# Performance work log

Measured on AMD Instinct MI355X. Metric: run time of the kernel, lower is better.

The kernel has to match this reference:

```python
import jax, jax.numpy as jnp
import numpy as np

B, H, T, D = 4, 16, 4096, 64
N_TASKS, K_LEN = 8, 128


def setup_inputs() -> dict:
    key = jax.random.key(0)
    ks = jax.random.split(key, 6)
    x = jax.random.normal(ks[0], (B, H, T, D), dtype=jnp.float32)
    q = jax.random.normal(ks[1], (B, H, T, D), dtype=jnp.float32)
    kv_k = jax.random.normal(ks[2], (N_TASKS, H, K_LEN, D), dtype=jnp.float32)
    kv_v = jax.random.normal(ks[3], (N_TASKS, H, K_LEN, D), dtype=jnp.float32)
    gates = jax.random.uniform(ks[4], (N_TASKS,), dtype=jnp.float32)
    trk_id = jax.random.randint(ks[5], (B, T), 0, N_TASKS, dtype=jnp.int64)
    return {"x": x, "q": q, "kv_k": kv_k, "kv_v": kv_v, "gates": gates, "trk_id": trk_id}


def reference(x, q, kv_k, kv_v, gates, trk_id):
    # Faithful to ICLAdaptor.fn: per-task SDPA of each token's query against
    # that task's (k, v) adaptor memory, scaled by a learned gate, scattered
    # back by trk_id, residual-added to x. Ragged torch gather/scatter is
    # expressed as masked per-task dense attention (small fixed n_tasks loop).
    d = q.shape[-1]
    scale = jnp.asarray(1.0, q.dtype) / jnp.sqrt(jnp.asarray(d, q.dtype))
    n_tasks = kv_k.shape[0]
    dx = jnp.zeros_like(q)
    for i in range(n_tasks):
        # scores: [b, h, t, k_len]
        s = jnp.einsum('bhtd,hkd->bhtk', q, kv_k[i]) * scale
        a = jax.nn.softmax(s, axis=-1)
        o = jnp.einsum('bhtk,hkd->bhtd', a, kv_v[i]) * gates[i]
        mask = (trk_id == i)[:, None, :, None]  # [b,1,t,1]
        dx = dx + jnp.where(mask, o, jnp.zeros((), o.dtype))
    return x + dx
```

## Files before the change

### kernel.cpp

```cpp
#include <hip/hip_runtime.h>

#define B_   4
#define H_   16
#define T_   4096
#define D_   64
#define KL_  128
#define NT_  8
#define NTOK (B_ * T_)
#define CAP  4096

typedef __bf16 bf16;
typedef __attribute__((ext_vector_type(8))) __bf16 bf16x8;
typedef __attribute__((ext_vector_type(4))) __bf16 bf16x4;
typedef __attribute__((ext_vector_type(4))) float  floatx4;
typedef __attribute__((ext_vector_type(4))) unsigned int uint4v;

__global__ void zero_counts_k(int* __restrict__ ws) {
    if (threadIdx.x < NT_) ws[threadIdx.x] = 0;
}

__global__ void scatter_tokens_k(const int* __restrict__ trk, int* __restrict__ ws) {
    int* counts = ws;
    int* bucket = ws + NT_;
    int idx  = blockIdx.x * blockDim.x + threadIdx.x;
    int lane = threadIdx.x & 63;
    int task = (idx < NTOK) ? trk[idx] : -1;
    unsigned long long mymask = 0ull;
    int myCnt = 0;
#pragma unroll
    for (int i = 0; i < NT_; i++) {
        unsigned long long m = __ballot(task == i);
        if (task == i) mymask = m;
        if (lane == i) myCnt = (int)__popcll(m);
    }
    int b0 = 0;
    if (lane < NT_) b0 = atomicAdd(&counts[lane], myCnt);
    int myBase = __shfl(b0, (task < 0) ? 0 : task);
    if (idx < NTOK) {
        int pos = myBase + (int)__popcll(mymask & ((1ull << lane) - 1ull));
        bucket[task * CAP + pos] = idx;
    }
}

static __device__ __forceinline__ unsigned pk_bf16(float a, float b) {
    unsigned short ua = __builtin_bit_cast(unsigned short, (bf16)a);
    unsigned short ub = __builtin_bit_cast(unsigned short, (bf16)b);
    return (unsigned)ua | ((unsigned)ub << 16);
}

__global__ __launch_bounds__(256) void attn_k(
    const float* __restrict__ q,   const float* __restrict__ kvk,
    const float* __restrict__ kvv, const float* __restrict__ gates,
    const float* __restrict__ x,   float* __restrict__ out,
    const int* __restrict__ ws)
{
    __shared__ bf16 Kl[KL_ * D_];
    __shared__ bf16 Vt[D_ * KL_];

    const int task = blockIdx.z, h = blockIdx.y, chunk = blockIdx.x;
    const int cnt = ws[task];
    if (cnt == 0) return;
    const int* bucket = ws + NT_ + task * CAP;
    const float gate = gates[task];

    {
        const size_t kvbase = (size_t)(task * H_ + h) * (KL_ * D_ / 4);
        const float4* kf = (const float4*)kvk + kvbase;
        const float4* vf = (const float4*)kvv + kvbase;
#pragma unroll
        for (int it = 0; it < 8; it++) {
            int ii = it * 256 + threadIdx.x;
            int k = ii >> 4, d4 = ii & 15;
            float4 a = kf[ii];
            bf16x4 w; w[0]=(bf16)a.x; w[1]=(bf16)a.y; w[2]=(bf16)a.z; w[3]=(bf16)a.w;
            *(bf16x4*)&Kl[(k << 6) + (((d4 >> 1) ^ (k & 7)) << 3) + ((d4 & 1) << 2)] = w;
            float4 v = vf[ii];
            int d0 = d4 << 2, ku = k >> 3, kl = k & 7;
            Vt[(d0+0)*128 + ((ku ^ ((d0+0)&7))<<3) + kl] = (bf16)v.x;
            Vt[(d0+1)*128 + ((ku ^ ((d0+1)&7))<<3) + kl] = (bf16)v.y;
            Vt[(d0+2)*128 + ((ku ^ ((d0+2)&7))<<3) + kl] = (bf16)v.z;
            Vt[(d0+3)*128 + ((ku ^ ((d0+3)&7))<<3) + kl] = (bf16)v.w;
        }
    }
    __syncthreads();

    const int lane = threadIdx.x & 63;
    const int wave = threadIdx.x >> 6;
    const int c = lane & 15, quad = lane >> 4;
    const int cswz = c & 7;
    const int src_h0 = c + 16 * (( 2 * quad     ) & 3);
    const int src_h1 = c + 16 * (( 2 * quad + 1 ) & 3);
    const bool hiSel = ((quad >> 1) & 1) != 0;

    for (int ts = chunk * 4 + wave; ts * 16 < cnt; ts += 64) {
        const int slotc = ts * 16 + c;
        const int tokc  = bucket[slotc < cnt ? slotc : cnt - 1];

        bf16x8 aq[2];
        {
            int bb = tokc >> 12, tt = tokc & (T_ - 1);
            const float4* qf = (const float4*)q + ((size_t)((bb * H_ + h) * T_ + tt) * (D_ / 4));
#pragma unroll
            for (int dc = 0; dc < 2; dc++) {
                float4 f0 = qf[dc * 8 + quad * 2];
                float4 f1 = qf[dc * 8 + quad * 2 + 1];
                aq[dc][0]=(bf16)f0.x; aq[dc][1]=(bf16)f0.y; aq[dc][2]=(bf16)f0.z; aq[dc][3]=(bf16)f0.w;
                aq[dc][4]=(bf16)f1.x; aq[dc][5]=(bf16)f1.y; aq[dc][6]=(bf16)f1.z; aq[dc][7]=(bf16)f1.w;
            }
        }

        floatx4 sc[8];
#pragma unroll
        for (int nt = 0; nt < 8; nt++) { floatx4 z = {0.f,0.f,0.f,0.f}; sc[nt] = z; }
        __builtin_amdgcn_s_setprio(1);
#pragma unroll
        for (int dc = 0; dc < 2; dc++) {
#pragma unroll
            for (int nt = 0; nt < 8; nt++) {
                bf16x8 ak = *(const bf16x8*)&Kl[((nt * 16 + c) << 6) + (((4 * dc + quad) ^ cswz) << 3)];
                sc[nt] = __builtin_amdgcn_mfma_f32_16x16x32_bf16(ak, aq[dc], sc[nt], 0, 0, 0);
            }
        }
        __builtin_amdgcn_s_setprio(0);

        float m = -1e30f;
#pragma unroll
        for (int nt = 0; nt < 8; nt++)
#pragma unroll
            for (int r = 0; r < 4; r++) m = fmaxf(m, sc[nt][r]);
        m = fmaxf(m, __shfl_xor(m, 16));
        m = fmaxf(m, __shfl_xor(m, 32));
        float sum = 0.f;
#pragma unroll
        for (int nt = 0; nt < 8; nt++)
#pragma unroll
            for (int r = 0; r < 4; r++) {
                float p = exp2f((sc[nt][r] - m) * 0.18033688011112042f);
                sc[nt][r] = p;
                sum += p;
            }
        sum += __shfl_xor(sum, 16);
        sum += __shfl_xor(sum, 32);
        float ginv = gate / sum;

        unsigned pkv[8][2];
#pragma unroll
        for (int nt = 0; nt < 8; nt++) {
            pkv[nt][0] = pk_bf16(sc[nt][0], sc[nt][1]);
            pkv[nt][1] = pk_bf16(sc[nt][2], sc[nt][3]);
        }

        int base_r[4];
        float xr[4][4];
#pragma unroll
        for (int r = 0; r < 4; r++) {
            int tok = __shfl(tokc, quad * 4 + r);
            int b2 = tok >> 12, t2 = tok & (T_ - 1);
            base_r[r] = ((b2 * H_ + h) * T_ + t2) * D_;
            if (ts * 16 + quad * 4 + r < cnt) {
#pragma unroll
                for (int dt = 0; dt < 4; dt++) xr[r][dt] = x[base_r[r] + dt * 16 + c];
            }
        }

        floatx4 acc[4];
#pragma unroll
        for (int dt = 0; dt < 4; dt++) { floatx4 z = {0.f,0.f,0.f,0.f}; acc[dt] = z; }
#pragma unroll
        for (int kc = 0; kc < 4; kc++) {
            unsigned e0 = pkv[2*kc][0],   e1 = pkv[2*kc][1];
            unsigned o0 = pkv[2*kc+1][0], o1 = pkv[2*kc+1][1];
            unsigned a0e = __shfl(e0, src_h0), a0o = __shfl(o0, src_h0);
            unsigned a1e = __shfl(e1, src_h0), a1o = __shfl(o1, src_h0);
            unsigned a2e = __shfl(e0, src_h1), a2o = __shfl(o0, src_h1);
            unsigned a3e = __shfl(e1, src_h1), a3o = __shfl(o1, src_h1);
            uint4v uw;
            uw[0] = hiSel ? a0o : a0e;
            uw[1] = hiSel ? a1o : a1e;
            uw[2] = hiSel ? a2o : a2e;
            uw[3] = hiSel ? a3o : a3e;
            bf16x8 ap = __builtin_bit_cast(bf16x8, uw);
            __builtin_amdgcn_s_setprio(1);
#pragma unroll
            for (int dt = 0; dt < 4; dt++) {
                bf16x8 bv = *(const bf16x8*)&Vt[((dt * 16 + c) << 7) + (((4 * kc + quad) ^ cswz) << 3)];
                acc[dt] = __builtin_amdgcn_mfma_f32_16x16x32_bf16(ap, bv, acc[dt], 0, 0, 0);
            }
            __builtin_amdgcn_s_setprio(0);
        }

#pragma unroll
        for (int r = 0; r < 4; r++) {
            int slot = ts * 16 + quad * 4 + r;
            float scale = __shfl(ginv, quad * 4 + r);
            if (slot < cnt) {
#pragma unroll
                for (int dt = 0; dt < 4; dt++) {
                    int off = base_r[r] + dt * 16 + c;
                    out[off] = xr[r][dt] + acc[dt][r] * scale;
                }
            }
        }
    }
}

extern "C" void kernel_launch(void* const* d_in, const int* in_sizes, int n_in,
                              void* d_out, int out_size, void* d_ws, size_t ws_size,
                              hipStream_t stream) {
    const float* x     = (const float*)d_in[0];
    const float* q     = (const float*)d_in[1];
    const float* kvk   = (const float*)d_in[2];
    const float* kvv   = (const float*)d_in[3];
    const float* gates = (const float*)d_in[4];
    const int*   trk   = (const int*)d_in[5];
    float* out = (float*)d_out;
    int* ws = (int*)d_ws;

    zero_counts_k<<<1, 64, 0, stream>>>(ws);
    scatter_tokens_k<<<NTOK / 256, 256, 0, stream>>>(trk, ws);
    attn_k<<<dim3(16, H_, NT_), 256, 0, stream>>>(q, kvk, kvv, gates, x, out, ws);
}
```

Before: 214.4 us.

## Bucket tokens per 512-token window and loop tasks inside each attention block

```diff
diff --git a/kernel.cpp b/kernel.cpp
--- a/kernel.cpp
+++ b/kernel.cpp
@@ -7,7 +7,8 @@
 #define KL_  128
 #define NT_  8
 #define NTOK (B_ * T_)
-#define CAP  4096
+#define WIN  512
+#define NWIN (NTOK / WIN)
 
 typedef __bf16 bf16;
 typedef __attribute__((ext_vector_type(8))) __bf16 bf16x8;
@@ -15,16 +16,15 @@
 typedef __attribute__((ext_vector_type(4))) float  floatx4;
 typedef __attribute__((ext_vector_type(4))) unsigned int uint4v;
 
-__global__ void zero_counts_k(int* __restrict__ ws) {
-    if (threadIdx.x < NT_) ws[threadIdx.x] = 0;
-}
-
-__global__ void scatter_tokens_k(const int* __restrict__ trk, int* __restrict__ ws) {
-    int* counts = ws;
-    int* bucket = ws + NT_;
-    int idx  = blockIdx.x * blockDim.x + threadIdx.x;
-    int lane = threadIdx.x & 63;
-    int task = (idx < NTOK) ? trk[idx] : -1;
+__device__ int g_ws[NWIN * NT_ + NTOK];
+
+__global__ __launch_bounds__(512) void scatter_win_k(const int* __restrict__ trk) {
+    __shared__ int wcnt[8][NT_];
+    __shared__ int wbase[8][NT_];
+    const int w = blockIdx.x, tid = threadIdx.x;
+    const int wv = tid >> 6, lane = tid & 63;
+    const int tok = w * WIN + tid;
+    const int task = trk[tok];
     unsigned long long mymask = 0ull;
     int myCnt = 0;
 #pragma unroll
@@ -33,13 +33,22 @@
         if (task == i) mymask = m;
         if (lane == i) myCnt = (int)__popcll(m);
     }
-    int b0 = 0;
-    if (lane < NT_) b0 = atomicAdd(&counts[lane], myCnt);
-    int myBase = __shfl(b0, (task < 0) ? 0 : task);
-    if (idx < NTOK) {
-        int pos = myBase + (int)__popcll(mymask & ((1ull << lane) - 1ull));
-        bucket[task * CAP + pos] = idx;
+    if (lane < NT_) wcnt[wv][lane] = myCnt;
+    __syncthreads();
+    if (tid == 0) {
+        int base = 0;
+#pragma unroll
+        for (int i = 0; i < NT_; i++) {
+            g_ws[w * NT_ + i] = base;
+            int s = base;
+#pragma unroll
+            for (int v = 0; v < 8; v++) { wbase[v][i] = s; s += wcnt[v][i]; }
+            base = s;
+        }
     }
+    __syncthreads();
+    int pos = wbase[wv][task] + (int)__popcll(mymask & ((1ull << lane) - 1ull));
+    g_ws[NWIN * NT_ + w * WIN + pos] = tok;
 }
 
 static __device__ __forceinline__ unsigned pk_bf16(float a, float b) {
@@ -51,38 +60,13 @@
 __global__ __launch_bounds__(256) void attn_k(
     const float* __restrict__ q,   const float* __restrict__ kvk,
     const float* __restrict__ kvv, const float* __restrict__ gates,
-    const float* __restrict__ x,   float* __restrict__ out,
-    const int* __restrict__ ws)
+    const float* __restrict__ x,   float* __restrict__ out)
 {
     __shared__ bf16 Kl[KL_ * D_];
     __shared__ bf16 Vt[D_ * KL_];
 
-    const int task = blockIdx.z, h = blockIdx.y, chunk = blockIdx.x;
-    const int cnt = ws[task];
-    if (cnt == 0) return;
-    const int* bucket = ws + NT_ + task * CAP;
-    const float gate = gates[task];
-
-    {
-        const size_t kvbase = (size_t)(task * H_ + h) * (KL_ * D_ / 4);
-        const float4* kf = (const float4*)kvk + kvbase;
-        const float4* vf = (const float4*)kvv + kvbase;
-#pragma unroll
-        for (int it = 0; it < 8; it++) {
-            int ii = it * 256 + threadIdx.x;
-            int k = ii >> 4, d4 = ii & 15;
-            float4 a = kf[ii];
-            bf16x4 w; w[0]=(bf16)a.x; w[1]=(bf16)a.y; w[2]=(bf16)a.z; w[3]=(bf16)a.w;
-            *(bf16x4*)&Kl[(k << 6) + (((d4 >> 1) ^ (k & 7)) << 3) + ((d4 & 1) << 2)] = w;
-            float4 v = vf[ii];
-            int d0 = d4 << 2, ku = k >> 3, kl = k & 7;
-            Vt[(d0+0)*128 + ((ku ^ ((d0+0)&7))<<3) + kl] = (bf16)v.x;
-            Vt[(d0+1)*128 + ((ku ^ ((d0+1)&7))<<3) + kl] = (bf16)v.y;
-            Vt[(d0+2)*128 + ((ku ^ ((d0+2)&7))<<3) + kl] = (bf16)v.z;
-            Vt[(d0+3)*128 + ((ku ^ ((d0+3)&7))<<3) + kl] = (bf16)v.w;
-        }
-    }
-    __syncthreads();
+    const int w = blockIdx.x, h = blockIdx.y;
+    const int* wlist = g_ws + NWIN * NT_ + w * WIN;
 
     const int lane = threadIdx.x & 63;
     const int wave = threadIdx.x >> 6;
@@ -91,113 +75,151 @@
     const int src_h0 = c + 16 * (( 2 * quad     ) & 3);
     const int src_h1 = c + 16 * (( 2 * quad + 1 ) & 3);
     const bool hiSel = ((quad >> 1) & 1) != 0;
-
-    for (int ts = chunk * 4 + wave; ts * 16 < cnt; ts += 64) {
-        const int slotc = ts * 16 + c;
-        const int tokc  = bucket[slotc < cnt ? slotc : cnt - 1];
-
-        bf16x8 aq[2];
+    const float4* qbase = (const float4*)q;
+
+    int offs[NT_ + 1];
+#pragma unroll
+    for (int i = 0; i < NT_; i++) offs[i] = g_ws[w * NT_ + i];
+    offs[NT_] = WIN;
+
+    for (int task = 0; task < NT_; task++) {
+        const int off = offs[task];
+        const int cnt = offs[task + 1] - off;
+        if (cnt == 0) continue;
+        __syncthreads();
+
         {
-            int bb = tokc >> 12, tt = tokc & (T_ - 1);
-            const float4* qf = (const float4*)q + ((size_t)((bb * H_ + h) * T_ + tt) * (D_ / 4));
+            const size_t kvbase = (size_t)(task * H_ + h) * (KL_ * D_ / 4);
+            const float4* kf = (const float4*)kvk + kvbase;
+            const float4* vf = (const float4*)kvv + kvbase;
+#pragma unroll
+            for (int it = 0; it < 8; it++) {
+                int ii = it * 256 + threadIdx.x;
+                int k = ii >> 4, d4 = ii & 15;
+                float4 a = kf[ii];
+                bf16x4 wv4; wv4[0]=(bf16)a.x; wv4[1]=(bf16)a.y; wv4[2]=(bf16)a.z; wv4[3]=(bf16)a.w;
+                *(bf16x4*)&Kl[(k << 6) + (((d4 >> 1) ^ (k & 7)) << 3) + ((d4 & 1) << 2)] = wv4;
+                float4 v = vf[ii];
+                int d0 = d4 << 2, ku = k >> 3, kl = k & 7;
+                Vt[(d0+0)*128 + ((ku ^ ((d0+0)&7))<<3) + kl] = (bf16)v.x;
+                Vt[(d0+1)*128 + ((ku ^ ((d0+1)&7))<<3) + kl] = (bf16)v.y;
+                Vt[(d0+2)*128 + ((ku ^ ((d0+2)&7))<<3) + kl] = (bf16)v.z;
+                Vt[(d0+3)*128 + ((ku ^ ((d0+3)&7))<<3) + kl] = (bf16)v.w;
+            }
+        }
+        __syncthreads();
+
+        const float gate = gates[task];
+        const int ntiles = (cnt + 15) >> 4;
+
+        for (int tile = wave; tile < ntiles; tile += 4) {
+            int slot = off + tile * 16 + c;
+            int slmax = off + cnt - 1;
+            const int tokc = wlist[slot < slmax ? slot : slmax];
+
+            bf16x8 aq[2];
+            {
+                int bb = tokc >> 12, tt = tokc & (T_ - 1);
+                const float4* qf = qbase + ((size_t)((bb * H_ + h) * T_ + tt) * (D_ / 4));
+#pragma unroll
+                for (int dc = 0; dc < 2; dc++) {
+                    float4 f0 = qf[dc * 8 + quad * 2];
+                    float4 f1 = qf[dc * 8 + quad * 2 + 1];
+                    aq[dc][0]=(bf16)f0.x; aq[dc][1]=(bf16)f0.y; aq[dc][2]=(bf16)f0.z; aq[dc][3]=(bf16)f0.w;
+                    aq[dc][4]=(bf16)f1.x; aq[dc][5]=(bf16)f1.y; aq[dc][6]=(bf16)f1.z; aq[dc][7]=(bf16)f1.w;
+                }
+            }
+
+            floatx4 sc[8];
+#pragma unroll
+            for (int nt = 0; nt < 8; nt++) { floatx4 z = {0.f,0.f,0.f,0.f}; sc[nt] = z; }
+            __builtin_amdgcn_s_setprio(1);
 #pragma unroll
             for (int dc = 0; dc < 2; dc++) {
-                float4 f0 = qf[dc * 8 + quad * 2];
-                float4 f1 = qf[dc * 8 + quad * 2 + 1];
-                aq[dc][0]=(bf16)f0.x; aq[dc][1]=(bf16)f0.y; aq[dc][2]=(bf16)f0.z; aq[dc][3]=(bf16)f0.w;
-                aq[dc][4]=(bf16)f1.x; aq[dc][5]=(bf16)f1.y; aq[dc][6]=(bf16)f1.z; aq[dc][7]=(bf16)f1.w;
-            }
-        }
-
-        floatx4 sc[8];
-#pragma unroll
-        for (int nt = 0; nt < 8; nt++) { floatx4 z = {0.f,0.f,0.f,0.f}; sc[nt] = z; }
-        __builtin_amdgcn_s_setprio(1);
-#pragma unroll
-        for (int dc = 0; dc < 2; dc++) {
+#pragma unroll
+                for (int nt = 0; nt < 8; nt++) {
+                    bf16x8 ak = *(const bf16x8*)&Kl[((nt * 16 + c) << 6) + (((4 * dc + quad) ^ cswz) << 3)];
+                    sc[nt] = __builtin_amdgcn_mfma_f32_16x16x32_bf16(ak, aq[dc], sc[nt], 0, 0, 0);
+                }
+            }
+            __builtin_amdgcn_s_setprio(0);
+
+            float m = -1e30f;
+#pragma unroll
+            for (int nt = 0; nt < 8; nt++)
+#pragma unroll
+                for (int r = 0; r < 4; r++) m = fmaxf(m, sc[nt][r]);
+            m = fmaxf(m, __shfl_xor(m, 16));
+            m = fmaxf(m, __shfl_xor(m, 32));
+            float sum = 0.f;
+#pragma unroll
+            for (int nt = 0; nt < 8; nt++)
+#pragma unroll
+                for (int r = 0; r < 4; r++) {
+                    float p = exp2f((sc[nt][r] - m) * 0.18033688011112042f);
+                    sc[nt][r] = p;
+                    sum += p;
+                }
+            sum += __shfl_xor(sum, 16);
+            sum += __shfl_xor(sum, 32);
+            float ginv = gate / sum;
+
+            unsigned pkv[8][2];
 #pragma unroll
             for (int nt = 0; nt < 8; nt++) {
-                bf16x8 ak = *(const bf16x8*)&Kl[((nt * 16 + c) << 6) + (((4 * dc + quad) ^ cswz) << 3)];
-                sc[nt] = __builtin_amdgcn_mfma_f32_16x16x32_bf16(ak, aq[dc], sc[nt], 0, 0, 0);
-            }
-        }
-        __builtin_amdgcn_s_setprio(0);
-
-        float m = -1e30f;
-#pragma unroll
-        for (int nt = 0; nt < 8; nt++)
-#pragma unroll
-            for (int r = 0; r < 4; r++) m = fmaxf(m, sc[nt][r]);
-        m = fmaxf(m, __shfl_xor(m, 16));
-        m = fmaxf(m, __shfl_xor(m, 32));
-        float sum = 0.f;
-#pragma unroll
-        for (int nt = 0; nt < 8; nt++)
+                pkv[nt][0] = pk_bf16(sc[nt][0], sc[nt][1]);
+                pkv[nt][1] = pk_bf16(sc[nt][2], sc[nt][3]);
+            }
+
+            int base_r[4];
+            float xr[4][4];
 #pragma unroll
             for (int r = 0; r < 4; r++) {
-                float p = exp2f((sc[nt][r] - m) * 0.18033688011112042f);
-                sc[nt][r] = p;
-                sum += p;
-            }
-        sum += __shfl_xor(sum, 16);
-        sum += __shfl_xor(sum, 32);
-        float ginv = gate / sum;
-
-        unsigned pkv[8][2];
-#pragma unroll
-        for (int nt = 0; nt < 8; nt++) {
-            pkv[nt][0] = pk_bf16(sc[nt][0], sc[nt][1]);
-            pkv[nt][1] = pk_bf16(sc[nt][2], sc[nt][3]);
-        }
-
-        int base_r[4];
-        float xr[4][4];
-#pragma unroll
-        for (int r = 0; r < 4; r++) {
-            int tok = __shfl(tokc, quad * 4 + r);
-            int b2 = tok >> 12, t2 = tok & (T_ - 1);
-            base_r[r] = ((b2 * H_ + h) * T_ + t2) * D_;
-            if (ts * 16 + quad * 4 + r < cnt) {
-#pragma unroll
-                for (int dt = 0; dt < 4; dt++) xr[r][dt] = x[base_r[r] + dt * 16 + c];
-            }
-        }
-
-        floatx4 acc[4];
-#pragma unroll
-        for (int dt = 0; dt < 4; dt++) { floatx4 z = {0.f,0.f,0.f,0.f}; acc[dt] = z; }
-#pragma unroll
-        for (int kc = 0; kc < 4; kc++) {
-            unsigned e0 = pkv[2*kc][0],   e1 = pkv[2*kc][1];
-            unsigned o0 = pkv[2*kc+1][0], o1 = pkv[2*kc+1][1];
-            unsigned a0e = __shfl(e0, src_h0), a0o = __shfl(o0, src_h0);
-            unsigned a1e = __shfl(e1, src_h0), a1o = __shfl(o1, src_h0);
-            unsigned a2e = __shfl(e0, src_h1), a2o = __shfl(o0, src_h1);
-            unsigned a3e = __shfl(e1, src_h1), a3o = __shfl(o1, src_h1);
-            uint4v uw;
-            uw[0] = hiSel ? a0o : a0e;
-            uw[1] = hiSel ? a1o : a1e;
-            uw[2] = hiSel ? a2o : a2e;
-            uw[3] = hiSel ? a3o : a3e;
-            bf16x8 ap = __builtin_bit_cast(bf16x8, uw);
-            __builtin_amdgcn_s_setprio(1);
-#pragma unroll
-            for (int dt = 0; dt < 4; dt++) {
-                bf16x8 bv = *(const bf16x8*)&Vt[((dt * 16 + c) << 7) + (((4 * kc + quad) ^ cswz) << 3)];
-                acc[dt] = __builtin_amdgcn_mfma_f32_16x16x32_bf16(ap, bv, acc[dt], 0, 0, 0);
-            }
-            __builtin_amdgcn_s_setprio(0);
-        }
-
-#pragma unroll
-        for (int r = 0; r < 4; r++) {
-            int slot = ts * 16 + quad * 4 + r;
-            float scale = __shfl(ginv, quad * 4 + r);
-            if (slot < cnt) {
+                int tok = __shfl(tokc, quad * 4 + r);
+                int b2 = tok >> 12, t2 = tok & (T_ - 1);
+                base_r[r] = ((b2 * H_ + h) * T_ + t2) * D_;
+                if (tile * 16 + quad * 4 + r < cnt) {
+#pragma unroll
+                    for (int dt = 0; dt < 4; dt++) xr[r][dt] = x[base_r[r] + dt * 16 + c];
+                }
+            }
+
+            floatx4 acc[4];
+#pragma unroll
+            for (int dt = 0; dt < 4; dt++) { floatx4 z = {0.f,0.f,0.f,0.f}; acc[dt] = z; }
+#pragma unroll
+            for (int kc = 0; kc < 4; kc++) {
+                unsigned e0 = pkv[2*kc][0],   e1 = pkv[2*kc][1];
+                unsigned o0 = pkv[2*kc+1][0], o1 = pkv[2*kc+1][1];
+                unsigned a0e = __shfl(e0, src_h0), a0o = __shfl(o0, src_h0);
+                unsigned a1e = __shfl(e1, src_h0), a1o = __shfl(o1, src_h0);
+                unsigned a2e = __shfl(e0, src_h1), a2o = __shfl(o0, src_h1);
+                unsigned a3e = __shfl(e1, src_h1), a3o = __shfl(o1, src_h1);
+                uint4v uw;
+                uw[0] = hiSel ? a0o : a0e;
+                uw[1] = hiSel ? a1o : a1e;
+                uw[2] = hiSel ? a2o : a2e;
+                uw[3] = hiSel ? a3o : a3e;
+                bf16x8 ap = __builtin_bit_cast(bf16x8, uw);
+                __builtin_amdgcn_s_setprio(1);
 #pragma unroll
                 for (int dt = 0; dt < 4; dt++) {
-                    int off = base_r[r] + dt * 16 + c;
-                    out[off] = xr[r][dt] + acc[dt][r] * scale;
+                    bf16x8 bv = *(const bf16x8*)&Vt[((dt * 16 + c) << 7) + (((4 * kc + quad) ^ cswz) << 3)];
+                    acc[dt] = __builtin_amdgcn_mfma_f32_16x16x32_bf16(ap, bv, acc[dt], 0, 0, 0);
+                }
+                __builtin_amdgcn_s_setprio(0);
+            }
+
+#pragma unroll
+            for (int r = 0; r < 4; r++) {
+                int sl = tile * 16 + quad * 4 + r;
+                float scale = __shfl(ginv, quad * 4 + r);
+                if (sl < cnt) {
+#pragma unroll
+                    for (int dt = 0; dt < 4; dt++) {
+                        int off2 = base_r[r] + dt * 16 + c;
+                        out[off2] = xr[r][dt] + acc[dt][r] * scale;
+                    }
                 }
             }
         }
@@ -214,9 +236,8 @@
     const float* gates = (const float*)d_in[4];
     const int*   trk   = (const int*)d_in[5];
     float* out = (float*)d_out;
-    int* ws = (int*)d_ws;
-
-    zero_counts_k<<<1, 64, 0, stream>>>(ws);
-    scatter_tokens_k<<<NTOK / 256, 256, 0, stream>>>(trk, ws);
-    attn_k<<<dim3(16, H_, NT_), 256, 0, stream>>>(q, kvk, kvv, gates, x, out, ws);
-}
+    (void)d_ws; (void)ws_size;
+
+    scatter_win_k<<<NWIN, 512, 0, stream>>>(trk);
+    attn_k<<<dim3(NWIN, H_), 256, 0, stream>>>(q, kvk, kvv, gates, x, out);
+}
```

Measured after the change: 252.3 us. 17.7% more time.
